# Kernel optimization log

Measured on AMD Instinct MI355X. Metric: run time of the kernel, lower is better.

The kernel has to match this reference:

```python
import jax, jax.numpy as jnp
import numpy as np
import math

BN_EPS = 1e-5
L2_EPS = 1e-12
TEMPARATURE = 0.01
Q_IN_DIM = 256


def _masked_bn(y, mask, gamma, beta):
    # y: [S, L, D], mask: [S, L] float (1 = valid packed row).
    # Emulates BatchNorm1d (training mode) over the packed valid rows.
    m = mask[..., None]
    cnt = jnp.sum(mask)
    mean = jnp.sum(y * m, axis=(0, 1)) / cnt
    var = jnp.sum(jnp.square(y - mean) * m, axis=(0, 1)) / cnt  # biased var
    return (y - mean) * jax.lax.rsqrt(var + BN_EPS) * gamma + beta


def _ctx_proj(x, W, b, gamma, beta, mask, normalize):
    y = jnp.einsum('sld,od->slo', x, W) + b
    y = jax.nn.relu(_masked_bn(y, mask, gamma, beta))
    if normalize:
        n = jnp.linalg.norm(y, axis=-1, keepdims=True)
        y = y / jnp.maximum(n, L2_EPS)
    return y


def setup_inputs() -> dict:
    key = jax.random.key(0)
    ks = jax.random.split(key, 8)
    S, La, Lb = 256, 128, 512
    Dq, Dkv, Dqk, Dv = 256, 265, 512, 512
    A = jax.random.normal(ks[0], (S, La, Dq), jnp.float32)
    B = jax.random.normal(ks[1], (S, Lb, Dkv), jnp.float32)
    a_lens = jax.random.randint(ks[2], (S,), 1, La + 1, jnp.int32)
    b_lens = jax.random.randint(ks[3], (S,), 1, Lb + 1, jnp.int32)
    pk = jax.random.split(ks[4], 4)
    sc = 0.05
    return {
        'A': A, 'B': B, 'a_lens': a_lens, 'b_lens': b_lens,
        'Wq': sc * jax.random.normal(pk[0], (Dqk, Dq), jnp.float32),
        'bq': jnp.zeros((Dqk,), jnp.float32),
        'gq': jnp.ones((Dqk,), jnp.float32),
        'betaq': jnp.zeros((Dqk,), jnp.float32),
        'Wk': sc * jax.random.normal(pk[1], (Dqk, Dkv), jnp.float32),
        'bk': jnp.zeros((Dqk,), jnp.float32),
        'gk': jnp.ones((Dqk,), jnp.float32),
        'betak': jnp.zeros((Dqk,), jnp.float32),
        'Wv': sc * jax.random.normal(pk[2], (Dv, Dkv), jnp.float32),
        'bv': jnp.zeros((Dv,), jnp.float32),
        'gv': jnp.ones((Dv,), jnp.float32),
        'betav': jnp.zeros((Dv,), jnp.float32),
        'Wf': sc * jax.random.normal(pk[3], (Dq, Dv), jnp.float32),
        'bf': jnp.zeros((Dq,), jnp.float32),
        'gf': jnp.ones((Dq,), jnp.float32),
        'betaf': jnp.zeros((Dq,), jnp.float32),
    }


def reference(A, B, a_lens, b_lens,
              Wq, bq, gq, betaq,
              Wk, bk, gk, betak,
              Wv, bv, gv, betav,
              Wf, bf, gf, betaf):
    S, La, _ = A.shape
    Lb = B.shape[1]
    mask_a = (jnp.arange(La)[None, :] < a_lens[:, None]).astype(A.dtype)  # [S, La]
    mask_b = (jnp.arange(Lb)[None, :] < b_lens[:, None]).astype(B.dtype)  # [S, Lb]

    q = _ctx_proj(A, Wq, bq, gq, betaq, mask_a, True)   # [S, La, Dqk]
    k = _ctx_proj(B, Wk, bk, gk, betak, mask_b, True)   # [S, Lb, Dqk]
    v = _ctx_proj(B, Wv, bv, gv, betav, mask_b, True)   # [S, Lb, Dv]

    scaler = 1.0 / (TEMPARATURE * math.sqrt(Q_IN_DIM))
    scores = jnp.einsum('sad,sbd->sab', q, k) * scaler  # [S, La, Lb]
    scores = jnp.where(mask_b[:, None, :] > 0, scores, -1e30)
    w = jax.nn.softmax(scores, axis=-1)
    wv = jnp.einsum('sab,sbd->sad', w, v)               # [S, La, Dv]

    f = _ctx_proj(wv, Wf, bf, gf, betaf, mask_a, False)  # [S, La, Dq]
    return f * mask_a[..., None]
```

## Files before the change

kernel.cpp:

```cpp
#include <hip/hip_runtime.h>
#include <hip/hip_bf16.h>
#include <stdint.h>


typedef __attribute__((ext_vector_type(8))) short short8;
typedef __attribute__((ext_vector_type(4))) float floatx4;

__device__ __forceinline__ float bf2f(short h) {
    union { unsigned u; float f; } c;
    c.u = ((unsigned)(unsigned short)h) << 16;
    return c.f;
}
__device__ __forceinline__ short f2bf(float f) {
    union { float f; unsigned u; } c;
    c.f = f;
    unsigned u = c.u + 0x7fffu + ((c.u >> 16) & 1u);
    return (short)(u >> 16);
}

__device__ __forceinline__ void async_cp16(const short* g, short* l) {
    __builtin_amdgcn_global_load_lds(
        (const __attribute__((address_space(1))) unsigned int*)g,
        (__attribute__((address_space(3))) unsigned int*)l, 16, 0, 0);
}

__device__ __forceinline__ short8 cvt8load(const float* p) {
    float4 f0 = *(const float4*)(p);
    float4 f1 = *(const float4*)(p + 4);
    short8 r;
    r[0] = f2bf(f0.x); r[1] = f2bf(f0.y); r[2] = f2bf(f0.z); r[3] = f2bf(f0.w);
    r[4] = f2bf(f1.x); r[5] = f2bf(f1.y); r[6] = f2bf(f1.z); r[7] = f2bf(f1.w);
    return r;
}
__device__ __forceinline__ short8 cvt8guard(const float* row, int c0, int Kin) {
    short8 r;
#pragma unroll
    for (int j = 0; j < 8; j++) {
        int c = c0 + j;
        r[j] = (c < Kin) ? f2bf(row[c]) : (short)0;
    }
    return r;
}

__global__ __launch_bounds__(256) void cvt_pad(const float* __restrict__ in,
                                               short* __restrict__ out,
                                               int kin, int kout) {
    long row = blockIdx.x;
    const float* src = in + row * (long)kin;
    short* dst = out + row * (long)kout;
    for (int c = threadIdx.x; c < kout; c += 256)
        dst[c] = (c < kin) ? f2bf(src[c]) : (short)0;
}

__global__ __launch_bounds__(256) void cvt_padB(const float* __restrict__ in,
                                                short* __restrict__ out,
                                                int kin, int kout,
                                                const int* __restrict__ lens) {
    long row = blockIdx.x;
    int pos = (int)(row & 511), s = (int)(row >> 9);
    if (pos >= ((lens[s] + 127) & ~127)) return;
    const float* src = in + row * (long)kin;
    short* dst = out + row * (long)kout;
    for (int c = threadIdx.x; c < kout; c += 256)
        dst[c] = (c < kin) ? f2bf(src[c]) : (short)0;
}

__global__ __launch_bounds__(256, 2)
void gemm128x2(const short* __restrict__ X,
               const short* __restrict__ W0, const short* __restrict__ W1,
               const float* __restrict__ bias0, const float* __restrict__ bias1,
               short* __restrict__ Y0, short* __restrict__ Y1,
               float* __restrict__ st0, float* __restrict__ st1,
               int N, int Kp, const int* __restrict__ lens, int Lshift,
               int nShift)
{
    __shared__ short SH[36864];
    const int lin = blockIdx.x;
    const int xcd = lin & 7, sl = lin >> 3;
    const int nb = sl & ((1 << nShift) - 1);
    const int ms = sl >> nShift;
    const int m0 = (ms * 8 + xcd) * 128;
    if ((m0 & ((1 << Lshift) - 1)) >= lens[m0 >> Lshift]) return;
    const int n0 = nb * 128;

    const int tid = threadIdx.x;
    const int l = tid & 63, w = tid >> 6;
    const int quad = l >> 4, l15 = l & 15;
    const int wr = w & 1, wc = w >> 1;
    const int mo = wr * 64, no = wc * 64;

    floatx4 acc0[4][4], acc1[4][4];
#pragma unroll
    for (int i = 0; i < 4; i++)
#pragma unroll
        for (int j = 0; j < 4; j++) {
            acc0[i][j] = (floatx4){0.f, 0.f, 0.f, 0.f};
            acc1[i][j] = (floatx4){0.f, 0.f, 0.f, 0.f};
        }

    int srow[2], scolS[2];
#pragma unroll
    for (int c = 0; c < 2; c++) {
        int L = tid * 16 + c * 4096;
        int S = L ^ ((((L >> 6) ^ (L >> 8)) & 1) << 4)
                  ^ (((L >> 7) & 1) << 5)
                  ^ (((L >> 8) & 1) << 6);
        srow[c] = S >> 6;
        scolS[c] = (S & 48) >> 1;
    }
    const short* Xs[2];
    const short* W0s[2];
    const short* W1s[2];
#pragma unroll
    for (int c = 0; c < 2; c++) {
        Xs[c]  = X  + (long)(m0 + srow[c]) * Kp + scolS[c];
        W0s[c] = W0 + (long)(n0 + srow[c]) * Kp + scolS[c];
        W1s[c] = W1 + (long)(n0 + srow[c]) * Kp + scolS[c];
    }
    const int nsteps = Kp >> 5;

    int rsA[4], rsB[4];
#pragma unroll
    for (int i = 0; i < 4; i++) {
        int rA = mo + i * 16 + l15;
        int rB = no + i * 16 + l15;
        rsA[i] = (rA << 6) ^ ((rA & 7) << 4) ^ (quad << 4);
        rsB[i] = (rB << 6) ^ ((rB & 7) << 4) ^ (quad << 4);
    }

    auto stage = [&](int buf, int t) {
        short* At = SH + buf * 12288;
        short* B0t = At + 4096;
        short* B1t = At + 8192;
        const int ko = t * 32;
#pragma unroll
        for (int c = 0; c < 2; c++)
            async_cp16(Xs[c] + ko, At + c * 2048 + tid * 8);
#pragma unroll
        for (int c = 0; c < 2; c++)
            async_cp16(W0s[c] + ko, B0t + c * 2048 + tid * 8);
#pragma unroll
        for (int c = 0; c < 2; c++)
            async_cp16(W1s[c] + ko, B1t + c * 2048 + tid * 8);
    };

    stage(0, 0);
    if (nsteps > 1) stage(1, 1);
    if (nsteps > 2) stage(2, 2);

    int cur = 0;
    for (int t = 0; t < nsteps; t++) {
        if (t + 2 < nsteps)      asm volatile("s_waitcnt vmcnt(12)" ::: "memory");
        else if (t + 1 < nsteps) asm volatile("s_waitcnt vmcnt(6)" ::: "memory");
        else                     asm volatile("s_waitcnt vmcnt(0)" ::: "memory");
        __builtin_amdgcn_s_barrier();
        __builtin_amdgcn_sched_barrier(0);

        const char* At = (const char*)(SH + cur * 12288);
        const char* B0t = At + 8192;
        const char* B1t = At + 16384;
        short8 af[4], bfr[4];
#pragma unroll
        for (int i = 0; i < 4; i++)
            af[i] = *(const short8*)(At + rsA[i]);
#pragma unroll
        for (int j = 0; j < 4; j++)
            bfr[j] = *(const short8*)(B0t + rsB[j]);
#pragma unroll
        for (int i = 0; i < 4; i++)
#pragma unroll
            for (int j = 0; j < 4; j++)
                acc0[i][j] = __builtin_amdgcn_mfma_f32_16x16x32_bf16(af[i], bfr[j], acc0[i][j], 0, 0, 0);
#pragma unroll
        for (int j = 0; j < 4; j++)
            bfr[j] = *(const short8*)(B1t + rsB[j]);
#pragma unroll
        for (int i = 0; i < 4; i++)
#pragma unroll
            for (int j = 0; j < 4; j++)
                acc1[i][j] = __builtin_amdgcn_mfma_f32_16x16x32_bf16(af[i], bfr[j], acc1[i][j], 0, 0, 0);

        __builtin_amdgcn_sched_barrier(0);
        __builtin_amdgcn_s_barrier();
        if (t + 3 < nsteps) stage(cur, t + 3);
        cur = (cur == 2) ? 0 : cur + 1;
    }

    const int Lmask = (1 << Lshift) - 1;
    float msk[4][4];
#pragma unroll
    for (int i = 0; i < 4; i++)
#pragma unroll
        for (int r = 0; r < 4; r++) {
            int rg = m0 + mo + i * 16 + quad * 4 + r;
            msk[i][r] = ((rg & Lmask) < lens[rg >> Lshift]) ? 1.f : 0.f;
        }
    short* Cs = SH;

    auto epi = [&](floatx4 (&acc)[4][4], const float* bias, float* stats, short* Y) {
        float bv[4];
#pragma unroll
        for (int j = 0; j < 4; j++) bv[j] = bias[n0 + no + j * 16 + l15];
#pragma unroll
        for (int j = 0; j < 4; j++) {
            float ps = 0.f, pss = 0.f;
#pragma unroll
            for (int i = 0; i < 4; i++)
#pragma unroll
                for (int r = 0; r < 4; r++) {
                    float v = acc[i][j][r] + bv[j];
                    ps += v * msk[i][r];
                    pss += v * v * msk[i][r];
                }
            ps  += __shfl_xor(ps, 16, 64);  ps  += __shfl_xor(ps, 32, 64);
            pss += __shfl_xor(pss, 16, 64); pss += __shfl_xor(pss, 32, 64);
            if (l < 16) {
                atomicAdd(&stats[n0 + no + j * 16 + l15], ps);
                atomicAdd(&stats[N + n0 + no + j * 16 + l15], pss);
            }
        }
#pragma unroll
        for (int pass = 0; pass < 2; pass++) {
            __syncthreads();
            if (wr == pass) {
#pragma unroll
                for (int j = 0; j < 4; j++)
#pragma unroll
                    for (int i = 0; i < 4; i++)
#pragma unroll
                        for (int r = 0; r < 4; r++)
                            Cs[(i * 16 + quad * 4 + r) * 132 + no + j * 16 + l15] =
                                f2bf(acc[i][j][r] + bv[j]);
            }
            __syncthreads();
#pragma unroll
            for (int c = 0; c < 4; c++) {
                int e = c * 2048 + tid * 8;
                int row = e >> 7, col = e & 127;
                short8 vv = *(const short8*)(Cs + row * 132 + col);
                *(short8*)(Y + (long)(m0 + pass * 64 + row) * N + n0 + col) = vv;
            }
        }
    };
    epi(acc0, bias0, st0, Y0);
    epi(acc1, bias1, st1, Y1);
}

__global__ __launch_bounds__(256, 3)
void gemm128(const short* __restrict__ X,
             const short* __restrict__ W0, const short* __restrict__ W1,
             const float* __restrict__ bias0, const float* __restrict__ bias1,
             short* __restrict__ Y0, short* __restrict__ Y1,
             float* __restrict__ st0, float* __restrict__ st1,
             int N, int Kp, const int* __restrict__ lens, int Lshift,
             int nShift, int dual)
{
    __shared__ short SH[24576];
    const int lin = blockIdx.x;
    const int xcd = lin & 7, sl = lin >> 3;
    const int nb = sl & ((1 << nShift) - 1);
    const int ms = sl >> nShift;
    const int m0 = (ms * 8 + xcd) * 128;
    int g = 0, n0;
    if (dual) { g = nb & 1; n0 = (nb >> 1) * 128; } else { n0 = nb * 128; }
    const short* W    = g ? W1 : W0;
    const float* bias = g ? bias1 : bias0;
    short* Y          = g ? Y1 : Y0;
    float* stats      = g ? st1 : st0;

    const int tid = threadIdx.x;
    const int l = tid & 63, w = tid >> 6;
    const int quad = l >> 4, l15 = l & 15;
    const int wr = w & 1, wc = w >> 1;
    const int mo = wr * 64, no = wc * 64;

    floatx4 acc[4][4];
#pragma unroll
    for (int i = 0; i < 4; i++)
#pragma unroll
        for (int j = 0; j < 4; j++) acc[i][j] = (floatx4){0.f, 0.f, 0.f, 0.f};

    const int srow = tid >> 2;
    const int scol = (tid & 3) * 8;
    const short* Xs = X + (long)(m0 + srow) * Kp + scol;
    const short* Ws = W + (long)(n0 + srow) * Kp + scol;
    const long strideR = (long)64 * Kp;
    const int nsteps = Kp >> 5;

    auto stage = [&](int buf, int t) {
        short* At = SH + buf * 8192;
        short* Bt = At + 4096;
        const short* Xk = Xs + t * 32;
        const short* Wk = Ws + t * 32;
        async_cp16(Xk,           At + tid * 8);
        async_cp16(Xk + strideR, At + 2048 + tid * 8);
        async_cp16(Wk,           Bt + tid * 8);
        async_cp16(Wk + strideR, Bt + 2048 + tid * 8);
    };

    stage(0, 0);
    if (nsteps > 1) stage(1, 1);
    if (nsteps > 2) stage(2, 2);

    int cur = 0;
    for (int t = 0; t < nsteps; t++) {
        if (t + 2 < nsteps)      asm volatile("s_waitcnt vmcnt(8)" ::: "memory");
        else if (t + 1 < nsteps) asm volatile("s_waitcnt vmcnt(4)" ::: "memory");
        else                     asm volatile("s_waitcnt vmcnt(0)" ::: "memory");
        __builtin_amdgcn_s_barrier();
        __builtin_amdgcn_sched_barrier(0);

        const short* At = SH + cur * 8192;
        const short* Bt = At + 4096;
        short8 af[4], bfr[4];
#pragma unroll
        for (int i = 0; i < 4; i++)
            af[i] = *(const short8*)(At + (mo + i * 16 + l15) * 32 + quad * 8);
#pragma unroll
        for (int j = 0; j < 4; j++)
            bfr[j] = *(const short8*)(Bt + (no + j * 16 + l15) * 32 + quad * 8);
#pragma unroll
        for (int i = 0; i < 4; i++)
#pragma unroll
            for (int j = 0; j < 4; j++)
                acc[i][j] = __builtin_amdgcn_mfma_f32_16x16x32_bf16(af[i], bfr[j], acc[i][j], 0, 0, 0);

        __builtin_amdgcn_sched_barrier(0);
        __builtin_amdgcn_s_barrier();
        if (t + 3 < nsteps) stage(cur, t + 3);
        cur = (cur == 2) ? 0 : cur + 1;
    }

    const int Lmask = (1 << Lshift) - 1;
    float msk[4][4];
#pragma unroll
    for (int i = 0; i < 4; i++)
#pragma unroll
        for (int r = 0; r < 4; r++) {
            int rg = m0 + mo + i * 16 + quad * 4 + r;
            msk[i][r] = ((rg & Lmask) < lens[rg >> Lshift]) ? 1.f : 0.f;
        }
    float bv[4];
#pragma unroll
    for (int j = 0; j < 4; j++) bv[j] = bias[n0 + no + j * 16 + l15];

#pragma unroll
    for (int j = 0; j < 4; j++) {
        float ps = 0.f, pss = 0.f;
#pragma unroll
        for (int i = 0; i < 4; i++)
#pragma unroll
            for (int r = 0; r < 4; r++) {
                float v = acc[i][j][r] + bv[j];
                ps += v * msk[i][r];
                pss += v * v * msk[i][r];
            }
        ps  += __shfl_xor(ps, 16, 64);  ps  += __shfl_xor(ps, 32, 64);
        pss += __shfl_xor(pss, 16, 64); pss += __shfl_xor(pss, 32, 64);
        if (l < 16) {
            atomicAdd(&stats[n0 + no + j * 16 + l15], ps);
            atomicAdd(&stats[N + n0 + no + j * 16 + l15], pss);
        }
    }

    short* Cs = SH;
#pragma unroll
    for (int pass = 0; pass < 2; pass++) {
        __syncthreads();
        if (wr == pass) {
#pragma unroll
            for (int j = 0; j < 4; j++)
#pragma unroll
                for (int i = 0; i < 4; i++)
#pragma unroll
                    for (int r = 0; r < 4; r++)
                        Cs[(i * 16 + quad * 4 + r) * 132 + no + j * 16 + l15] =
                            f2bf(acc[i][j][r] + bv[j]);
        }
        __syncthreads();
#pragma unroll
        for (int c = 0; c < 4; c++) {
            int e = c * 2048 + tid * 8;
            int row = e >> 7, col = e & 127;
            short8 vv = *(const short8*)(Cs + row * 132 + col);
            *(short8*)(Y + (long)(m0 + pass * 64 + row) * N + n0 + col) = vv;
        }
    }
}

template<bool XBF16, bool KAL>
__global__ __launch_bounds__(256, 2)
void gemm_bt(const void* __restrict__ Xp, const float* __restrict__ W,
             const float* __restrict__ bias, short* __restrict__ Y,
             int N, int Kin, int Kp, float* __restrict__ stats,
             const int* __restrict__ lens, int Lshift)
{
    __shared__ short At[128 * 32];
    __shared__ short Bt[128 * 32];
    const int m0 = blockIdx.x * 128;
    const int n0 = blockIdx.y * 128;
    const int tid = threadIdx.x;
    const int w = tid >> 6, l = tid & 63;
    const int quad = l >> 4, l15 = l & 15;
    const int mo = (w & 1) * 64, no = (w >> 1) * 64;

    floatx4 acc[4][4];
#pragma unroll
    for (int i = 0; i < 4; i++)
#pragma unroll
        for (int j = 0; j < 4; j++) acc[i][j] = (floatx4){0.f, 0.f, 0.f, 0.f};

    const int srow = tid >> 2;
    const int sc8 = (tid & 3) * 8;

    for (int k0 = 0; k0 < Kp; k0 += 32) {
        __syncthreads();
        const int c0 = k0 + sc8;
        short8 a0, a1, b0, b1;
        if (XBF16) {
            const short* X = (const short*)Xp;
            a0 = *(const short8*)(X + (long)(m0 + srow) * Kp + c0);
            a1 = *(const short8*)(X + (long)(m0 + 64 + srow) * Kp + c0);
        } else {
            const float* X = (const float*)Xp;
            if (KAL) {
                a0 = cvt8load(X + (long)(m0 + srow) * Kin + c0);
                a1 = cvt8load(X + (long)(m0 + 64 + srow) * Kin + c0);
            } else {
                a0 = cvt8guard(X + (long)(m0 + srow) * Kin, c0, Kin);
                a1 = cvt8guard(X + (long)(m0 + 64 + srow) * Kin, c0, Kin);
            }
        }
        if (KAL) {
            b0 = cvt8load(W + (long)(n0 + srow) * Kin + c0);
            b1 = cvt8load(W + (long)(n0 + 64 + srow) * Kin + c0);
        } else {
            b0 = cvt8guard(W + (long)(n0 + srow) * Kin, c0, Kin);
            b1 = cvt8guard(W + (long)(n0 + 64 + srow) * Kin, c0, Kin);
        }
        *(short8*)(At + srow * 32 + sc8) = a0;
        *(short8*)(At + (64 + srow) * 32 + sc8) = a1;
        *(short8*)(Bt + srow * 32 + sc8) = b0;
        *(short8*)(Bt + (64 + srow) * 32 + sc8) = b1;
        __syncthreads();
        short8 af[4], bfr[4];
#pragma unroll
        for (int i = 0; i < 4; i++) {
            af[i]  = *(const short8*)(At + (mo + i * 16 + l15) * 32 + quad * 8);
            bfr[i] = *(const short8*)(Bt + (no + i * 16 + l15) * 32 + quad * 8);
        }
#pragma unroll
        for (int i = 0; i < 4; i++)
#pragma unroll
            for (int j = 0; j < 4; j++)
                acc[i][j] = __builtin_amdgcn_mfma_f32_16x16x32_bf16(af[i], bfr[j], acc[i][j], 0, 0, 0);
    }

    const int Lmask = (1 << Lshift) - 1;
    float msk[4][4];
#pragma unroll
    for (int i = 0; i < 4; i++)
#pragma unroll
        for (int r = 0; r < 4; r++) {
            int rg = m0 + mo + i * 16 + quad * 4 + r;
            msk[i][r] = ((rg & Lmask) < lens[rg >> Lshift]) ? 1.f : 0.f;
        }
#pragma unroll
    for (int j = 0; j < 4; j++) {
        int colj = n0 + no + j * 16 + l15;
        float bvs = bias[colj];
        float ps = 0.f, pss = 0.f;
#pragma unroll
        for (int i = 0; i < 4; i++)
#pragma unroll
            for (int r = 0; r < 4; r++) {
                int rg = m0 + mo + i * 16 + quad * 4 + r;
                float v = acc[i][j][r] + bvs;
                Y[(long)rg * N + colj] = f2bf(v);
                ps += v * msk[i][r];
                pss += v * v * msk[i][r];
            }
        ps  += __shfl_xor(ps, 16, 64);  ps  += __shfl_xor(ps, 32, 64);
        pss += __shfl_xor(pss, 16, 64); pss += __shfl_xor(pss, 32, 64);
        if (l < 16) {
            atomicAdd(&stats[colj], ps);
            atomicAdd(&stats[N + colj], pss);
        }
    }
}

__global__ void finalize_stats(float* __restrict__ stats, const float* __restrict__ g,
                               const float* __restrict__ beta,
                               const int* __restrict__ lens, int C)
{
    __shared__ int lred[256];
    int t = threadIdx.x;
    if (t < 256) lred[t] = lens[t];
    __syncthreads();
    for (int s2 = 128; s2 > 0; s2 >>= 1) {
        if (t < s2) lred[t] += lred[t + s2];
        __syncthreads();
    }
    float cnt = (float)lred[0];
    if (t < C) {
        float mean = stats[t] / cnt;
        float var = fmaxf(stats[C + t] / cnt - mean * mean, 0.f);
        float a = rsqrtf(var + 1e-5f) * g[t];
        stats[t] = a;
        stats[C + t] = beta[t] - mean * a;
    }
}

__global__ __launch_bounds__(256)
void apply_norm512(short* __restrict__ Y, const float* __restrict__ stats)
{
    int w = threadIdx.x >> 6, l = threadIdx.x & 63;
    long row = (long)blockIdx.x * 4 + w;
    short8 yv = *(const short8*)(Y + row * 512 + l * 8);
    float v[8];
    float ss = 0.f;
#pragma unroll
    for (int i = 0; i < 8; i++) {
        int c = l * 8 + i;
        float t = fmaxf(bf2f(yv[i]) * stats[c] + stats[512 + c], 0.f);
        v[i] = t;
        ss += t * t;
    }
#pragma unroll
    for (int off = 1; off < 64; off <<= 1) ss += __shfl_xor(ss, off, 64);
    float scl = 1.f / fmaxf(sqrtf(ss), 1e-12f);
    short8 o;
#pragma unroll
    for (int i = 0; i < 8; i++) o[i] = f2bf(v[i] * scl);
    *(short8*)(Y + row * 512 + l * 8) = o;
}

__global__ __launch_bounds__(256)
void apply_norm512_len(short* __restrict__ Y, const float* __restrict__ stats,
                       const int* __restrict__ lens)
{
    int bid = blockIdx.x;
    if (((bid & 127) * 4) >= lens[bid >> 7]) return;
    int w = threadIdx.x >> 6, l = threadIdx.x & 63;
    long row = (long)bid * 4 + w;
    short8 yv = *(const short8*)(Y + row * 512 + l * 8);
    float v[8];
    float ss = 0.f;
#pragma unroll
    for (int i = 0; i < 8; i++) {
        int c = l * 8 + i;
        float t = fmaxf(bf2f(yv[i]) * stats[c] + stats[512 + c], 0.f);
        v[i] = t;
        ss += t * t;
    }
#pragma unroll
    for (int off = 1; off < 64; off <<= 1) ss += __shfl_xor(ss, off, 64);
    float scl = 1.f / fmaxf(sqrtf(ss), 1e-12f);
    short8 o;
#pragma unroll
    for (int i = 0; i < 8; i++) o[i] = f2bf(v[i] * scl);
    *(short8*)(Y + row * 512 + l * 8) = o;
}

template<int NT>
__device__ __forceinline__ void attn_body(
    short* __restrict__ tile, short* __restrict__ Pw,
    const short* __restrict__ qbase, const short* __restrict__ kbase,
    const short* __restrict__ vbase, short* __restrict__ wvbase,
    int blen, int tid, int quad, int l15, int wvStride)
{
    const int sr = tid >> 3;
    const int scg = (tid & 7) * 8;

    short8 qf[16];
#pragma unroll
    for (int kk = 0; kk < 16; kk++) qf[kk] = *(const short8*)(qbase + kk * 32);

    floatx4 sc[2 * NT];
#pragma unroll
    for (int i = 0; i < 2 * NT; i++) sc[i] = (floatx4){0.f, 0.f, 0.f, 0.f};

#pragma unroll
    for (int bt2 = 0; bt2 < NT; ++bt2) {
        __syncthreads();
        const short* krow = kbase + (long)(bt2 * 32 + sr) * 512;
#pragma unroll
        for (int i = 0; i < 2; i++) {
            short8 t0 = *(const short8*)(krow + i * 256 + scg);
            short8 t1 = *(const short8*)(krow + i * 256 + 64 + scg);
            short8 t2 = *(const short8*)(krow + i * 256 + 128 + scg);
            short8 t3 = *(const short8*)(krow + i * 256 + 192 + scg);
            *(short8*)(&tile[sr * 520 + i * 256 + scg]) = t0;
            *(short8*)(&tile[sr * 520 + i * 256 + 64 + scg]) = t1;
            *(short8*)(&tile[sr * 520 + i * 256 + 128 + scg]) = t2;
            *(short8*)(&tile[sr * 520 + i * 256 + 192 + scg]) = t3;
        }
        __syncthreads();
#pragma unroll
        for (int kk = 0; kk < 16; kk++) {
            short8 f0 = *(const short8*)(&tile[l15 * 520 + kk * 32 + quad * 8]);
            short8 f1 = *(const short8*)(&tile[(16 + l15) * 520 + kk * 32 + quad * 8]);
            sc[bt2 * 2]     = __builtin_amdgcn_mfma_f32_16x16x32_bf16(qf[kk], f0, sc[bt2 * 2], 0, 0, 0);
            sc[bt2 * 2 + 1] = __builtin_amdgcn_mfma_f32_16x16x32_bf16(qf[kk], f1, sc[bt2 * 2 + 1], 0, 0, 0);
        }
    }

    const float scaler = 6.25f;
    float mrow[4] = {-__builtin_inff(), -__builtin_inff(), -__builtin_inff(), -__builtin_inff()};
#pragma unroll
    for (int bt = 0; bt < 2 * NT; ++bt) {
        bool valid = (bt * 16 + l15) < blen;
#pragma unroll
        for (int r = 0; r < 4; r++) {
            float v2 = valid ? sc[bt][r] * scaler : -__builtin_inff();
            sc[bt][r] = v2;
            mrow[r] = fmaxf(mrow[r], v2);
        }
    }
#pragma unroll
    for (int r = 0; r < 4; r++) {
#pragma unroll
        for (int off = 1; off < 16; off <<= 1)
            mrow[r] = fmaxf(mrow[r], __shfl_xor(mrow[r], off, 64));
    }
    float ssum[4] = {0.f, 0.f, 0.f, 0.f};
#pragma unroll
    for (int bt = 0; bt < 2 * NT; ++bt)
#pragma unroll
        for (int r = 0; r < 4; r++) {
            float p = __expf(sc[bt][r] - mrow[r]);
            sc[bt][r] = p;
            ssum[r] += p;
        }
#pragma unroll
    for (int r = 0; r < 4; r++) {
#pragma unroll
        for (int off = 1; off < 16; off <<= 1) ssum[r] += __shfl_xor(ssum[r], off, 64);
        ssum[r] = 1.f / ssum[r];
    }

    short8 pf[NT];
#pragma unroll
    for (int kk = 0; kk < NT; kk++) {
#pragma unroll
        for (int half = 0; half < 2; half++)
#pragma unroll
            for (int r = 0; r < 4; r++)
                Pw[(quad * 4 + r) * 40 + half * 16 + l15] = f2bf(sc[kk * 2 + half][r] * ssum[r]);
        pf[kk] = *(const short8*)(&Pw[l15 * 40 + quad * 8]);
    }

    for (int dt = 0; dt < 16; ++dt) {
        __syncthreads();
#pragma unroll
        for (int round = 0; round < 2; round++) {
            int b = round * 256 + tid;
            if (NT == 16 || b < NT * 32) {
                const short* vr = vbase + (long)b * 512 + dt * 32;
                short8 x0 = *(const short8*)(vr);
                short8 x1 = *(const short8*)(vr + 8);
                short8 x2 = *(const short8*)(vr + 16);
                short8 x3 = *(const short8*)(vr + 24);
#pragma unroll
                for (int j = 0; j < 8; j++) {
                    tile[j * 520 + b]        = x0[j];
                    tile[(8 + j) * 520 + b]  = x1[j];
                    tile[(16 + j) * 520 + b] = x2[j];
                    tile[(24 + j) * 520 + b] = x3[j];
                }
            }
        }
        __syncthreads();
        floatx4 o0 = (floatx4){0.f, 0.f, 0.f, 0.f};
        floatx4 o1 = (floatx4){0.f, 0.f, 0.f, 0.f};
#pragma unroll
        for (int kk = 0; kk < NT; kk++) {
            short8 f0 = *(const short8*)(&tile[l15 * 520 + kk * 32 + quad * 8]);
            short8 f1 = *(const short8*)(&tile[(16 + l15) * 520 + kk * 32 + quad * 8]);
            o0 = __builtin_amdgcn_mfma_f32_16x16x32_bf16(pf[kk], f0, o0, 0, 0, 0);
            o1 = __builtin_amdgcn_mfma_f32_16x16x32_bf16(pf[kk], f1, o1, 0, 0, 0);
        }
#pragma unroll
        for (int r = 0; r < 4; r++) {
            wvbase[(long)r * wvStride + dt * 32 + l15]      = f2bf(o0[r]);
            wvbase[(long)r * wvStride + dt * 32 + 16 + l15] = f2bf(o1[r]);
        }
    }
}

__global__ __launch_bounds__(256)
void attention(const short* __restrict__ q, const short* __restrict__ k,
               const short* __restrict__ v, const int* __restrict__ b_lens,
               const int* __restrict__ a_lens,
               short* __restrict__ wv, int wvStride)
{
    __shared__ short tile[32 * 520];
    __shared__ short Pscr[4][16 * 40];
    const int lin = blockIdx.x;
    const int xcd = lin & 7, sl = lin >> 3;
    const int a0 = (sl & 1) * 64;
    const int s = (sl >> 1) * 8 + xcd;
    const int tid = threadIdx.x;
    const int w = tid >> 6, l = tid & 63;
    const int quad = l >> 4, l15 = l & 15;
    const int blen = b_lens[s];

    if (a_lens[s] <= a0) {
        short8 z = (short8){0, 0, 0, 0, 0, 0, 0, 0};
        short* wz = wv + (long)(s * 128 + a0) * wvStride;
        const int total = 64 * wvStride;
        for (int e = tid * 8; e < total; e += 2048)
            *(short8*)(wz + e) = z;
        return;
    }

    const short* qbase = q + ((long)(s * 128 + a0 + w * 16 + l15)) * 512 + quad * 8;
    const short* kbase = k + (long)s * 512 * 512;
    const short* vbase = v + (long)s * 512 * 512;
    short* wvbase = wv + (long)(s * 128 + a0 + w * 16 + quad * 4) * wvStride;
    short* Pw = Pscr[w];

    const int grp = (blen + 127) >> 7;
    if (grp == 1)
        attn_body<4>(tile, Pw, qbase, kbase, vbase, wvbase, blen, tid, quad, l15, wvStride);
    else if (grp == 2)
        attn_body<8>(tile, Pw, qbase, kbase, vbase, wvbase, blen, tid, quad, l15, wvStride);
    else if (grp == 3)
        attn_body<12>(tile, Pw, qbase, kbase, vbase, wvbase, blen, tid, quad, l15, wvStride);
    else
        attn_body<16>(tile, Pw, qbase, kbase, vbase, wvbase, blen, tid, quad, l15, wvStride);

    if (wvStride > 512) {
        int r = tid >> 2, cb = (tid & 3) * 16;
        short8 z = (short8){0, 0, 0, 0, 0, 0, 0, 0};
        short* pz = wv + (long)(s * 128 + a0 + r) * wvStride + 512 + cb;
        *(short8*)(pz) = z;
        *(short8*)(pz + 8) = z;
    }
}

__global__ __launch_bounds__(256)
void apply_f(const short* __restrict__ Yf, const float* __restrict__ stats,
             const int* __restrict__ a_lens, float* __restrict__ out)
{
    const long total = (long)32768 * 256;
    for (long e = (long)blockIdx.x * 256 + threadIdx.x; e < total; e += (long)gridDim.x * 256) {
        int c = (int)(e & 255);
        long row = e >> 8;
        int sI = (int)(row >> 7), pos = (int)(row & 127);
        float v = fmaxf(bf2f(Yf[e]) * stats[c] + stats[256 + c], 0.f);
        out[e] = (pos < a_lens[sI]) ? v : 0.f;
    }
}

extern "C" void kernel_launch(void* const* d_in, const int* in_sizes, int n_in,
                              void* d_out, int out_size, void* d_ws, size_t ws_size,
                              hipStream_t stream)
{
    (void)in_sizes; (void)n_in; (void)out_size;
    const float* A     = (const float*)d_in[0];
    const float* B     = (const float*)d_in[1];
    const int* a_lens  = (const int*)d_in[2];
    const int* b_lens  = (const int*)d_in[3];
    const float* Wq    = (const float*)d_in[4];
    const float* bq    = (const float*)d_in[5];
    const float* gq    = (const float*)d_in[6];
    const float* betaq = (const float*)d_in[7];
    const float* Wk    = (const float*)d_in[8];
    const float* bk    = (const float*)d_in[9];
    const float* gk    = (const float*)d_in[10];
    const float* betak = (const float*)d_in[11];
    const float* Wv    = (const float*)d_in[12];
    const float* bv    = (const float*)d_in[13];
    const float* gv    = (const float*)d_in[14];
    const float* betav = (const float*)d_in[15];
    const float* Wf    = (const float*)d_in[16];
    const float* bfp   = (const float*)d_in[17];
    const float* gf    = (const float*)d_in[18];
    const float* betaf = (const float*)d_in[19];
    float* out = (float*)d_out;
    char* base = (char*)d_ws;

    const size_t oWqb = 0;
    const size_t oWkb = oWqb + 294912;
    const size_t oWvb = oWkb + 294912;
    const size_t oWfb = oWvb + 294912;
    const size_t oBbf = oWfb + 294912;
    const size_t oQb  = oBbf + 75497472;
    const size_t oYv  = oQb + 33554432;
    const size_t oKb  = oYv + 134217728;
    const size_t oSt  = oKb + 134217728;
    const size_t FAST_NEED = oSt + 16384;

    if (ws_size >= FAST_NEED) {
        short* Wqb = (short*)(base + oWqb);
        short* Wkb = (short*)(base + oWkb);
        short* Wvb = (short*)(base + oWvb);
        short* Wfb = (short*)(base + oWfb);
        short* Bbf = (short*)(base + oBbf);
        short* qb  = (short*)(base + oQb);
        short* Yv  = (short*)(base + oYv);
        short* kb  = (short*)(base + oKb);
        short* Abf = (short*)(base + oKb);
        short* wvb = (short*)(base + oBbf);
        short* Yf  = (short*)(base + oQb);
        float* stQ = (float*)(base + oSt);
        float* stK = stQ + 1024;
        float* stV = stQ + 2048;
        float* stF = stQ + 3072;

        hipMemsetAsync(stQ, 0, 16384, stream);

        cvt_pad<<<32768, 256, 0, stream>>>(A, Abf, 256, 288);
        cvt_padB<<<131072, 256, 0, stream>>>(B, Bbf, 265, 288, b_lens);
        cvt_pad<<<512, 256, 0, stream>>>(Wq, Wqb, 256, 288);
        cvt_pad<<<512, 256, 0, stream>>>(Wk, Wkb, 265, 288);
        cvt_pad<<<512, 256, 0, stream>>>(Wv, Wvb, 265, 288);
        cvt_pad<<<256, 256, 0, stream>>>(Wf, Wfb, 512, 576);

        gemm128<<<1024, 256, 0, stream>>>(
            Abf, Wqb, Wqb, bq, bq, qb, qb, stQ, stQ, 512, 288, a_lens, 7, 2, 0);
        gemm128x2<<<4096, 256, 0, stream>>>(
            Bbf, Wvb, Wkb, bv, bk, Yv, kb, stV, stK, 512, 288, b_lens, 9, 2);

        finalize_stats<<<1, 512, 0, stream>>>(stV, gv, betav, b_lens, 512);
        finalize_stats<<<1, 512, 0, stream>>>(stK, gk, betak, b_lens, 512);
        finalize_stats<<<1, 512, 0, stream>>>(stQ, gq, betaq, a_lens, 512);
        apply_norm512_len<<<32768, 256, 0, stream>>>(Yv, stV, b_lens);
        apply_norm512_len<<<32768, 256, 0, stream>>>(kb, stK, b_lens);
        apply_norm512<<<8192, 256, 0, stream>>>(qb, stQ);

        attention<<<512, 256, 0, stream>>>(qb, kb, Yv, b_lens, a_lens, wvb, 576);

        gemm128<<<512, 256, 0, stream>>>(
            wvb, Wfb, Wfb, bfp, bfp, Yf, Yf, stF, stF, 256, 576, a_lens, 7, 1, 0);
        finalize_stats<<<1, 512, 0, stream>>>(stF, gf, betaf, a_lens, 256);
        apply_f<<<8192, 256, 0, stream>>>(Yf, stF, a_lens, out);
        return;
    }

    short* qb  = (short*)(base);
    short* Yv  = (short*)(base + 33554432);
    short* kb  = (short*)(base + 33554432 + 134217728);
    short* wvb = (short*)(base + 33554432 + 2L * 134217728);
    float* stQ = (float*)(base + 2L * 33554432 + 2L * 134217728);
    float* stK = stQ + 1024;
    float* stV = stQ + 2048;
    float* stF = stQ + 3072;
    short* Yf  = qb;

    hipMemsetAsync(stQ, 0, 16384, stream);

    gemm_bt<false, true><<<dim3(256, 4), 256, 0, stream>>>(
        A, Wq, bq, qb, 512, 256, 256, stQ, a_lens, 7);
    gemm_bt<false, false><<<dim3(1024, 4), 256, 0, stream>>>(
        B, Wv, bv, Yv, 512, 265, 288, stV, b_lens, 9);
    finalize_stats<<<1, 512, 0, stream>>>(stV, gv, betav, b_lens, 512);
    apply_norm512<<<32768, 256, 0, stream>>>(Yv, stV);
    gemm_bt<false, false><<<dim3(1024, 4), 256, 0, stream>>>(
        B, Wk, bk, kb, 512, 265, 288, stK, b_lens, 9);
    finalize_stats<<<1, 512, 0, stream>>>(stK, gk, betak, b_lens, 512);
    apply_norm512<<<32768, 256, 0, stream>>>(kb, stK);
    finalize_stats<<<1, 512, 0, stream>>>(stQ, gq, betaq, a_lens, 512);
    apply_norm512<<<8192, 256, 0, stream>>>(qb, stQ);
    attention<<<512, 256, 0, stream>>>(qb, kb, Yv, b_lens, a_lens, wvb, 512);
    gemm_bt<true, true><<<dim3(256, 2), 256, 0, stream>>>(
        wvb, Wf, bfp, Yf, 256, 512, 512, stF, a_lens, 7);
    finalize_stats<<<1, 512, 0, stream>>>(stF, gf, betaf, a_lens, 256);
    apply_f<<<8192, 256, 0, stream>>>(Yf, stF, a_lens, out);
}
```

Measured before the change: 712.4 us.

## Replace tiled projection GEMMs with persistent ticket-scheduled kernel keeping X row-tile in LDS

Replaces the 2D-tiled Q and fused K/V projection GEMM launches with a persistent 512-thread kernel. Each block takes 128-row M tiles from an atomic ticket counter, loads the whole K-extent of the X tile into LDS once, and loops over all N tiles (and both weight matrices in dual mode) while streaming weight slices through a 3-buffer ring. The aim is to cut redundant X reloads and skip padded tiles through dynamic scheduling. In exchange each block uses more LDS, the N tiles are processed serially per M tile, the pipeline is shallower with a barrier each sub-step, and the Q GEMM has only 256 tiles spread over 256 persistent blocks.

After: 816.4 us. 1.15x slower.

```diff
diff --git a/kernel.cpp b/kernel.cpp
--- a/kernel.cpp
+++ b/kernel.cpp
@@ -65,185 +65,166 @@
         dst[c] = (c < kin) ? f2bf(src[c]) : (short)0;
 }
 
-__global__ __launch_bounds__(256, 2)
-void gemm128x2(const short* __restrict__ X,
-               const short* __restrict__ W0, const short* __restrict__ W1,
-               const float* __restrict__ bias0, const float* __restrict__ bias1,
-               short* __restrict__ Y0, short* __restrict__ Y1,
-               float* __restrict__ st0, float* __restrict__ st1,
-               int N, int Kp, const int* __restrict__ lens, int Lshift,
-               int nShift)
-{
-    __shared__ short SH[36864];
-    const int lin = blockIdx.x;
-    const int xcd = lin & 7, sl = lin >> 3;
-    const int nb = sl & ((1 << nShift) - 1);
-    const int ms = sl >> nShift;
-    const int m0 = (ms * 8 + xcd) * 128;
-    if ((m0 & ((1 << Lshift) - 1)) >= lens[m0 >> Lshift]) return;
-    const int n0 = nb * 128;
+__global__ __launch_bounds__(512, 2)
+void gemm_persist(const short* __restrict__ X,
+                  const short* __restrict__ W0, const short* __restrict__ W1,
+                  const float* __restrict__ bias0, const float* __restrict__ bias1,
+                  short* __restrict__ Y0, short* __restrict__ Y1,
+                  float* __restrict__ st0, float* __restrict__ st1,
+                  int N, int Kp, const int* __restrict__ lens, int Lshift,
+                  int nTiles, int dual, int* __restrict__ ticket)
+{
+    __shared__ short SH[49152];
+    __shared__ int mtile_sh;
+    short* Xlds = SH;
+    short* Wlds = SH + 36864;
 
     const int tid = threadIdx.x;
     const int l = tid & 63, w = tid >> 6;
     const int quad = l >> 4, l15 = l & 15;
     const int wr = w & 1, wc = w >> 1;
-    const int mo = wr * 64, no = wc * 64;
-
-    floatx4 acc0[4][4], acc1[4][4];
-#pragma unroll
-    for (int i = 0; i < 4; i++)
-#pragma unroll
-        for (int j = 0; j < 4; j++) {
-            acc0[i][j] = (floatx4){0.f, 0.f, 0.f, 0.f};
-            acc1[i][j] = (floatx4){0.f, 0.f, 0.f, 0.f};
-        }
-
-    int srow[2], scolS[2];
-#pragma unroll
-    for (int c = 0; c < 2; c++) {
-        int L = tid * 16 + c * 4096;
+    const int mo = wr * 64, no32 = wc * 32;
+    const int nsub = Kp >> 5;
+    const int npass = (N >> 7) << dual;
+    const int Lmask = (1 << Lshift) - 1;
+
+    int srow, scolS;
+    {
+        int L = tid * 16;
         int S = L ^ ((((L >> 6) ^ (L >> 8)) & 1) << 4)
                   ^ (((L >> 7) & 1) << 5)
                   ^ (((L >> 8) & 1) << 6);
-        srow[c] = S >> 6;
-        scolS[c] = (S & 48) >> 1;
-    }
-    const short* Xs[2];
-    const short* W0s[2];
-    const short* W1s[2];
-#pragma unroll
-    for (int c = 0; c < 2; c++) {
-        Xs[c]  = X  + (long)(m0 + srow[c]) * Kp + scolS[c];
-        W0s[c] = W0 + (long)(n0 + srow[c]) * Kp + scolS[c];
-        W1s[c] = W1 + (long)(n0 + srow[c]) * Kp + scolS[c];
-    }
-    const int nsteps = Kp >> 5;
-
-    int rsA[4], rsB[4];
+        srow = S >> 6;
+        scolS = (S & 48) >> 1;
+    }
+    int rsA[4], rsB[2];
 #pragma unroll
     for (int i = 0; i < 4; i++) {
         int rA = mo + i * 16 + l15;
-        int rB = no + i * 16 + l15;
         rsA[i] = (rA << 6) ^ ((rA & 7) << 4) ^ (quad << 4);
-        rsB[i] = (rB << 6) ^ ((rB & 7) << 4) ^ (quad << 4);
-    }
-
-    auto stage = [&](int buf, int t) {
-        short* At = SH + buf * 12288;
-        short* B0t = At + 4096;
-        short* B1t = At + 8192;
-        const int ko = t * 32;
-#pragma unroll
-        for (int c = 0; c < 2; c++)
-            async_cp16(Xs[c] + ko, At + c * 2048 + tid * 8);
-#pragma unroll
-        for (int c = 0; c < 2; c++)
-            async_cp16(W0s[c] + ko, B0t + c * 2048 + tid * 8);
-#pragma unroll
-        for (int c = 0; c < 2; c++)
-            async_cp16(W1s[c] + ko, B1t + c * 2048 + tid * 8);
-    };
-
-    stage(0, 0);
-    if (nsteps > 1) stage(1, 1);
-    if (nsteps > 2) stage(2, 2);
-
-    int cur = 0;
-    for (int t = 0; t < nsteps; t++) {
-        if (t + 2 < nsteps)      asm volatile("s_waitcnt vmcnt(12)" ::: "memory");
-        else if (t + 1 < nsteps) asm volatile("s_waitcnt vmcnt(6)" ::: "memory");
-        else                     asm volatile("s_waitcnt vmcnt(0)" ::: "memory");
-        __builtin_amdgcn_s_barrier();
-        __builtin_amdgcn_sched_barrier(0);
-
-        const char* At = (const char*)(SH + cur * 12288);
-        const char* B0t = At + 8192;
-        const char* B1t = At + 16384;
-        short8 af[4], bfr[4];
+    }
+#pragma unroll
+    for (int j = 0; j < 2; j++) {
+        int rB = no32 + j * 16 + l15;
+        rsB[j] = (rB << 6) ^ ((rB & 7) << 4) ^ (quad << 4);
+    }
+
+    for (;;) {
+        __syncthreads();
+        if (tid == 0) mtile_sh = atomicAdd(ticket, 1);
+        __syncthreads();
+        const int mt = mtile_sh;
+        if (mt >= nTiles) break;
+        const int m0 = mt * 128;
+        if ((m0 & Lmask) >= lens[m0 >> Lshift]) continue;
+
+        const short* Xb = X + (long)(m0 + srow) * Kp + scolS;
+        for (int t = 0; t < nsub; t++)
+            async_cp16(Xb + t * 32, Xlds + t * 4096 + tid * 8);
+
+        float msk[4][4];
 #pragma unroll
         for (int i = 0; i < 4; i++)
-            af[i] = *(const short8*)(At + rsA[i]);
-#pragma unroll
-        for (int j = 0; j < 4; j++)
-            bfr[j] = *(const short8*)(B0t + rsB[j]);
-#pragma unroll
-        for (int i = 0; i < 4; i++)
-#pragma unroll
-            for (int j = 0; j < 4; j++)
-                acc0[i][j] = __builtin_amdgcn_mfma_f32_16x16x32_bf16(af[i], bfr[j], acc0[i][j], 0, 0, 0);
-#pragma unroll
-        for (int j = 0; j < 4; j++)
-            bfr[j] = *(const short8*)(B1t + rsB[j]);
-#pragma unroll
-        for (int i = 0; i < 4; i++)
-#pragma unroll
-            for (int j = 0; j < 4; j++)
-                acc1[i][j] = __builtin_amdgcn_mfma_f32_16x16x32_bf16(af[i], bfr[j], acc1[i][j], 0, 0, 0);
-
-        __builtin_amdgcn_sched_barrier(0);
-        __builtin_amdgcn_s_barrier();
-        if (t + 3 < nsteps) stage(cur, t + 3);
-        cur = (cur == 2) ? 0 : cur + 1;
-    }
-
-    const int Lmask = (1 << Lshift) - 1;
-    float msk[4][4];
-#pragma unroll
-    for (int i = 0; i < 4; i++)
-#pragma unroll
-        for (int r = 0; r < 4; r++) {
-            int rg = m0 + mo + i * 16 + quad * 4 + r;
-            msk[i][r] = ((rg & Lmask) < lens[rg >> Lshift]) ? 1.f : 0.f;
-        }
-    short* Cs = SH;
-
-    auto epi = [&](floatx4 (&acc)[4][4], const float* bias, float* stats, short* Y) {
-        float bv[4];
-#pragma unroll
-        for (int j = 0; j < 4; j++) bv[j] = bias[n0 + no + j * 16 + l15];
-#pragma unroll
-        for (int j = 0; j < 4; j++) {
-            float ps = 0.f, pss = 0.f;
+#pragma unroll
+            for (int r = 0; r < 4; r++) {
+                int rg = m0 + mo + i * 16 + quad * 4 + r;
+                msk[i][r] = ((rg & Lmask) < lens[rg >> Lshift]) ? 1.f : 0.f;
+            }
+
+        for (int p = 0; p < npass; p++) {
+            const int nb = dual ? (p >> 1) : p;
+            const int g  = dual ? (p & 1) : 0;
+            const short* W    = g ? W1 : W0;
+            const float* bias = g ? bias1 : bias0;
+            short* Y          = g ? Y1 : Y0;
+            float* stats      = g ? st1 : st0;
+            const int n0 = nb * 128;
+            const short* Wb = W + (long)(n0 + srow) * Kp + scolS;
+
+            floatx4 acc[4][2];
 #pragma unroll
             for (int i = 0; i < 4; i++)
 #pragma unroll
-                for (int r = 0; r < 4; r++) {
-                    float v = acc[i][j][r] + bv[j];
-                    ps += v * msk[i][r];
-                    pss += v * v * msk[i][r];
+                for (int j = 0; j < 2; j++) acc[i][j] = (floatx4){0.f, 0.f, 0.f, 0.f};
+
+            for (int t = 0; t < 3; t++)
+                async_cp16(Wb + t * 32, Wlds + t * 4096 + tid * 8);
+
+            for (int t = 0; t < nsub; t++) {
+                if (t + 2 < nsub)      asm volatile("s_waitcnt vmcnt(2)" ::: "memory");
+                else if (t + 1 < nsub) asm volatile("s_waitcnt vmcnt(1)" ::: "memory");
+                else                   asm volatile("s_waitcnt vmcnt(0)" ::: "memory");
+                __builtin_amdgcn_s_barrier();
+                __builtin_amdgcn_sched_barrier(0);
+
+                const char* Xt = (const char*)Xlds + t * 8192;
+                const char* Wt = (const char*)Wlds + (t % 3) * 8192;
+                short8 af[4], bfr[2];
+#pragma unroll
+                for (int i = 0; i < 4; i++)
+                    af[i] = *(const short8*)(Xt + rsA[i]);
+#pragma unroll
+                for (int j = 0; j < 2; j++)
+                    bfr[j] = *(const short8*)(Wt + rsB[j]);
+#pragma unroll
+                for (int i = 0; i < 4; i++)
+#pragma unroll
+                    for (int j = 0; j < 2; j++)
+                        acc[i][j] = __builtin_amdgcn_mfma_f32_16x16x32_bf16(af[i], bfr[j], acc[i][j], 0, 0, 0);
+
+                __builtin_amdgcn_sched_barrier(0);
+                __builtin_amdgcn_s_barrier();
+                if (t + 3 < nsub)
+                    async_cp16(Wb + (t + 3) * 32, Wlds + ((t + 3) % 3) * 4096 + tid * 8);
+            }
+
+            float bv[2];
+#pragma unroll
+            for (int j = 0; j < 2; j++) bv[j] = bias[n0 + no32 + j * 16 + l15];
+#pragma unroll
+            for (int j = 0; j < 2; j++) {
+                float ps = 0.f, pss = 0.f;
+#pragma unroll
+                for (int i = 0; i < 4; i++)
+#pragma unroll
+                    for (int r = 0; r < 4; r++) {
+                        float v = acc[i][j][r] + bv[j];
+                        ps += v * msk[i][r];
+                        pss += v * v * msk[i][r];
+                    }
+                ps  += __shfl_xor(ps, 16, 64);  ps  += __shfl_xor(ps, 32, 64);
+                pss += __shfl_xor(pss, 16, 64); pss += __shfl_xor(pss, 32, 64);
+                if (l < 16) {
+                    atomicAdd(&stats[n0 + no32 + j * 16 + l15], ps);
+                    atomicAdd(&stats[N + n0 + no32 + j * 16 + l15], pss);
                 }
-            ps  += __shfl_xor(ps, 16, 64);  ps  += __shfl_xor(ps, 32, 64);
-            pss += __shfl_xor(pss, 16, 64); pss += __shfl_xor(pss, 32, 64);
-            if (l < 16) {
-                atomicAdd(&stats[n0 + no + j * 16 + l15], ps);
-                atomicAdd(&stats[N + n0 + no + j * 16 + l15], pss);
             }
-        }
-#pragma unroll
-        for (int pass = 0; pass < 2; pass++) {
-            __syncthreads();
-            if (wr == pass) {
-#pragma unroll
-                for (int j = 0; j < 4; j++)
-#pragma unroll
-                    for (int i = 0; i < 4; i++)
-#pragma unroll
-                        for (int r = 0; r < 4; r++)
-                            Cs[(i * 16 + quad * 4 + r) * 132 + no + j * 16 + l15] =
-                                f2bf(acc[i][j][r] + bv[j]);
+            short* Cs = Wlds;
+#pragma unroll
+            for (int P = 0; P < 2; P++) {
+                __syncthreads();
+                if (wr == P) {
+#pragma unroll
+                    for (int j = 0; j < 2; j++)
+#pragma unroll
+                        for (int i = 0; i < 4; i++)
+#pragma unroll
+                            for (int r = 0; r < 4; r++)
+                                Cs[(i * 16 + quad * 4 + r) * 132 + no32 + j * 16 + l15] =
+                                    f2bf(acc[i][j][r] + bv[j]);
+                }
+                __syncthreads();
+#pragma unroll
+                for (int c = 0; c < 2; c++) {
+                    int e = c * 4096 + tid * 8;
+                    int row = e >> 7, col = e & 127;
+                    short8 vv = *(const short8*)(Cs + row * 132 + col);
+                    *(short8*)(Y + (long)(m0 + P * 64 + row) * N + n0 + col) = vv;
+                }
             }
             __syncthreads();
-#pragma unroll
-            for (int c = 0; c < 4; c++) {
-                int e = c * 2048 + tid * 8;
-                int row = e >> 7, col = e & 127;
-                short8 vv = *(const short8*)(Cs + row * 132 + col);
-                *(short8*)(Y + (long)(m0 + pass * 64 + row) * N + n0 + col) = vv;
-            }
-        }
-    };
-    epi(acc0, bias0, st0, Y0);
-    epi(acc1, bias1, st1, Y1);
+        }
+    }
 }
 
 __global__ __launch_bounds__(256, 3)
@@ -808,6 +789,8 @@
         float* stK = stQ + 1024;
         float* stV = stQ + 2048;
         float* stF = stQ + 3072;
+        int* ctrKV = (int*)(base + oSt + 14336);
+        int* ctrQ  = ctrKV + 1;
 
         hipMemsetAsync(stQ, 0, 16384, stream);
 
@@ -818,10 +801,12 @@
         cvt_pad<<<512, 256, 0, stream>>>(Wv, Wvb, 265, 288);
         cvt_pad<<<256, 256, 0, stream>>>(Wf, Wfb, 512, 576);
 
-        gemm128<<<1024, 256, 0, stream>>>(
-            Abf, Wqb, Wqb, bq, bq, qb, qb, stQ, stQ, 512, 288, a_lens, 7, 2, 0);
-        gemm128x2<<<4096, 256, 0, stream>>>(
-            Bbf, Wvb, Wkb, bv, bk, Yv, kb, stV, stK, 512, 288, b_lens, 9, 2);
+        gemm_persist<<<256, 512, 0, stream>>>(
+            Abf, Wqb, Wqb, bq, bq, qb, qb, stQ, stQ, 512, 288, a_lens, 7,
+            256, 0, ctrQ);
+        gemm_persist<<<256, 512, 0, stream>>>(
+            Bbf, Wvb, Wkb, bv, bk, Yv, kb, stV, stK, 512, 288, b_lens, 9,
+            1024, 1, ctrKV);
 
         finalize_stats<<<1, 512, 0, stream>>>(stV, gv, betav, b_lens, 512);
         finalize_stats<<<1, 512, 0, stream>>>(stK, gk, betak, b_lens, 512);
```
